# Kernel optimization log

Hardware: AMD Instinct MI355X
Metric: run time of the kernel (lower is better)

The kernel has to match this reference:

```python
import jax, jax.numpy as jnp
import numpy as np

DIM = 256
HEADS = 4
HEAD_DIM = DIM // HEADS  # 64
SCALE = (DIM / HEADS) ** -0.5
EPS = 1e-5


def layer_norm(x, g, b):
    mu = jnp.mean(x, axis=-1, keepdims=True)
    var = jnp.mean(jnp.square(x - mu), axis=-1, keepdims=True)
    return (x - mu) * jax.lax.rsqrt(var + EPS) * g + b


def setup_inputs() -> dict:
    key = jax.random.key(0)
    ks = jax.random.split(key, 8)
    B, N, C = 2, 64 * 64, DIM
    H = 4 * DIM  # mlp hidden
    s = lambda fan: 1.0 / np.sqrt(fan)
    return {
        "x": jax.random.normal(ks[0], (B, N, C), jnp.float32),
        "w_qkv": jax.random.normal(ks[1], (C, 3 * C), jnp.float32) * s(C),
        "w_ao": jax.random.normal(ks[2], (C, C), jnp.float32) * s(C),
        "b_ao": jnp.zeros((C,), jnp.float32),
        "g_ao": jnp.ones((C,), jnp.float32),
        "be_ao": jnp.zeros((C,), jnp.float32),
        "g1": jnp.ones((C,), jnp.float32),
        "be1": jnp.zeros((C,), jnp.float32),
        "w_fc1": jax.random.normal(ks[3], (C, H), jnp.float32) * s(C),
        "b_fc1": jnp.zeros((H,), jnp.float32),
        "w_fc2": jax.random.normal(ks[4], (H, C), jnp.float32) * s(H),
        "b_fc2": jnp.zeros((C,), jnp.float32),
        "g2": jnp.ones((C,), jnp.float32),
        "be2": jnp.zeros((C,), jnp.float32),
    }


def reference(x, w_qkv, w_ao, b_ao, g_ao, be_ao, g1, be1,
              w_fc1, b_fc1, w_fc2, b_fc2, g2, be2):
    b, n, c = x.shape
    shortcut = x

    # --- LinearAttention ---
    qkv = x @ w_qkv  # [b, n, 3c]
    qkv = qkv.reshape(b, n, 3, HEADS, HEAD_DIM).transpose(2, 0, 3, 1, 4)  # [3,b,h,n,d]
    q, k, v = qkv[0], qkv[1], qkv[2]
    k = jax.nn.softmax(k, axis=-2)  # softmax over sequence dim
    q = q * SCALE
    context = jnp.einsum('bhid,bhjd->bhij', k, v)   # [b,h,n,n]
    out = jnp.einsum('bhij,bhid->bhjd', context, q)  # [b,h,n,d]
    out = out.reshape(b, n, c)  # faithful to torch reshape (no transpose)
    attn_out = layer_norm(out @ w_ao + b_ao, g_ao, be_ao)

    # --- block residuals ---
    h = shortcut + layer_norm(attn_out, g1, be1)
    mlp = jax.nn.gelu(h @ w_fc1 + b_fc1) @ w_fc2 + b_fc2
    h = h + layer_norm(mlp, g2, be2)
    return shortcut + h
```

## Files before the change

kernel.cpp:

```cpp
#include <hip/hip_runtime.h>

typedef __attribute__((ext_vector_type(8))) short short8;
typedef __attribute__((ext_vector_type(4))) float f32x4;

#define EPSF 1e-5f
#define NSEQ 4096
#define R_TOT 8192

__device__ __forceinline__ float bf2f(unsigned short u){
  union { unsigned int i; float f; } v; v.i = ((unsigned int)u) << 16; return v.f;
}
__device__ __forceinline__ unsigned short f2bf(float f){
  union { float f; unsigned int i; } v; v.f = f;
  unsigned int u = v.i;
  u += 0x7FFFu + ((u >> 16) & 1u);
  return (unsigned short)(u >> 16);
}
__device__ __forceinline__ float wsum(float v){
  #pragma unroll
  for (int o = 32; o > 0; o >>= 1) v += __shfl_xor(v, o, 64);
  return v;
}
__device__ __forceinline__ float gelu_tanh(float x){
  float y = 0.7978845608028654f * (x + 0.044715f * x * x * x);
  float e = __expf(2.0f * y);
  float th = 1.0f - 2.0f / (e + 1.0f);
  return 0.5f * x * (1.0f + th);
}
__device__ __forceinline__ void gload_lds16(const unsigned short* g, unsigned short* l){
  __builtin_amdgcn_global_load_lds(
      (const __attribute__((address_space(1))) unsigned int*)g,
      (__attribute__((address_space(3))) unsigned int*)l, 16, 0, 0);
}

__global__ void k_prep(const float* __restrict__ x, unsigned short* __restrict__ xbf,
                       const float* __restrict__ w_qkv, const float* __restrict__ w_ao,
                       const float* __restrict__ w_fc1, const float* __restrict__ w_fc2,
                       unsigned short* __restrict__ oq, unsigned short* __restrict__ oa,
                       unsigned short* __restrict__ o1, unsigned short* __restrict__ o2)
{
  int bid = blockIdx.x;
  const int t = threadIdx.x;
  if (bid < 2048){
    int i = (bid * 256 + t) * 4;
    float4 v = *(const float4*)(x + i);
    ushort4 o;
    o.x = f2bf(v.x); o.y = f2bf(v.y); o.z = f2bf(v.z); o.w = f2bf(v.w);
    *(ushort4*)(xbf + i) = o;
    return;
  }
  bid -= 2048;
  const float* in; unsigned short* out; int rows, cols, tid;
  if (bid < 48)      { in = w_qkv; out = oq; rows = 256;  cols = 768;  tid = bid; }
  else if (bid < 64) { in = w_ao;  out = oa; rows = 256;  cols = 256;  tid = bid - 48; }
  else if (bid < 128){ in = w_fc1; out = o1; rows = 256;  cols = 1024; tid = bid - 64; }
  else               { in = w_fc2; out = o2; rows = 1024; cols = 256;  tid = bid - 128; }
  const int tC = cols >> 6;
  const int r0 = (tid / tC) * 64, c0 = (tid % tC) * 64;
  __shared__ float tile[64][68];
  const int i = t >> 4, j4 = (t & 15) * 4;
  #pragma unroll
  for (int p = 0; p < 4; p++){
    float4 v = *(const float4*)(in + (size_t)(r0 + i + p * 16) * cols + c0 + j4);
    tile[i + p * 16][j4 + 0] = v.x; tile[i + p * 16][j4 + 1] = v.y;
    tile[i + p * 16][j4 + 2] = v.z; tile[i + p * 16][j4 + 3] = v.w;
  }
  __syncthreads();
  #pragma unroll
  for (int p = 0; p < 4; p++){
    int ci = i + p * 16;
    ushort4 o;
    o.x = f2bf(tile[j4 + 0][ci]); o.y = f2bf(tile[j4 + 1][ci]);
    o.z = f2bf(tile[j4 + 2][ci]); o.w = f2bf(tile[j4 + 3][ci]);
    *(ushort4*)(out + (size_t)(c0 + ci) * rows + r0 + j4) = o;
  }
}

template<int BM, int BN, bool HAS_BIAS, bool DO_GELU, bool OUT_BF16>
__global__ __launch_bounds__(256) void k_gemm(const unsigned short* __restrict__ A,
                       const unsigned short* __restrict__ BT,
                       const float* __restrict__ bias,
                       float* __restrict__ Cf,
                       unsigned short* __restrict__ Cb,
                       int M, int N, int K)
{
  constexpr int BK = 64;
  constexpr int FM = BM / 32, FN = BN / 32;
  __shared__ unsigned short As[2][BM * BK];
  __shared__ unsigned short Bs[2][BN * BK];
  const int t  = threadIdx.x;
  const int l  = t & 63;
  const int w  = t >> 6;
  const int wm = w >> 1, wn = w & 1;
  const int lr = l & 15, kq = l >> 4;
  const int m0 = blockIdx.y * BM, n0 = blockIdx.x * BN;

  f32x4 acc[FM][FN];
  #pragma unroll
  for (int i = 0; i < FM; i++)
    #pragma unroll
    for (int j = 0; j < FN; j++) acc[i][j] = (f32x4){0.f, 0.f, 0.f, 0.f};

  const int crow = l >> 3, ccolE = (l & 7) * 8;
  const int nk = K / BK;

  auto stage = [&](int s, int bsel){
    #pragma unroll
    for (int c = w; c < BM / 8; c += 4)
      gload_lds16(A  + (size_t)(m0 + c * 8 + crow) * K + s * BK + ccolE, &As[bsel][c * 512]);
    #pragma unroll
    for (int c = w; c < BN / 8; c += 4)
      gload_lds16(BT + (size_t)(n0 + c * 8 + crow) * K + s * BK + ccolE, &Bs[bsel][c * 512]);
  };

  stage(0, 0);
  __syncthreads();
  for (int s = 0; s < nk; ++s){
    const int cur = s & 1;
    if (s + 1 < nk) stage(s + 1, cur ^ 1);
    #pragma unroll
    for (int kk = 0; kk < BK; kk += 32){
      short8 af[FM], bfr[FN];
      #pragma unroll
      for (int i = 0; i < FM; i++)
        af[i]  = *(const short8*)&As[cur][(wm * (BM / 2) + i * 16 + lr) * 64 + kk + kq * 8];
      #pragma unroll
      for (int j = 0; j < FN; j++)
        bfr[j] = *(const short8*)&Bs[cur][(wn * (BN / 2) + j * 16 + lr) * 64 + kk + kq * 8];
      #pragma unroll
      for (int i = 0; i < FM; i++)
        #pragma unroll
        for (int j = 0; j < FN; j++)
          acc[i][j] = __builtin_amdgcn_mfma_f32_16x16x32_bf16(af[i], bfr[j], acc[i][j], 0, 0, 0);
    }
    __syncthreads();
  }

  const int row0 = m0 + wm * (BM / 2);
  const int col0 = n0 + wn * (BN / 2);
  #pragma unroll
  for (int i = 0; i < FM; i++){
    #pragma unroll
    for (int j = 0; j < FN; j++){
      #pragma unroll
      for (int r = 0; r < 4; r++){
        int row = row0 + i * 16 + kq * 4 + r;
        int col = col0 + j * 16 + lr;
        float v = acc[i][j][r];
        if (HAS_BIAS) v += bias[col];
        if (DO_GELU)  v = gelu_tanh(v);
        if (OUT_BF16) Cb[(size_t)row * N + col] = f2bf(v);
        else          Cf[(size_t)row * N + col] = v;
      }
    }
  }
}

#define NPAD 72
__global__ __launch_bounds__(256) void k_msum(const unsigned short* __restrict__ qkv,
                                              float* __restrict__ Spart,
                                              float* __restrict__ dsum_part)
{
  __shared__ unsigned short kT[64 * NPAD];
  __shared__ unsigned short qT[80 * NPAD];
  const int t = threadIdx.x;
  const int sl = blockIdx.x;
  const int bh = blockIdx.y;
  const int b = bh >> 2, h = bh & 3;
  const int e4 = (t & 15) * 4;
  const int col = (t >> 4) * 4;
  {
    int n = sl * 64 + col;
    const unsigned short* rp = qkv + (size_t)(b * NSEQ + n) * 768 + h * 64 + e4;
    ushort4 q0 = *(const ushort4*)(rp);
    ushort4 q1 = *(const ushort4*)(rp + 768);
    ushort4 q2 = *(const ushort4*)(rp + 1536);
    ushort4 q3 = *(const ushort4*)(rp + 2304);
    ushort4 k0 = *(const ushort4*)(rp + 256);
    ushort4 k1 = *(const ushort4*)(rp + 1024);
    ushort4 k2 = *(const ushort4*)(rp + 1792);
    ushort4 k3 = *(const ushort4*)(rp + 2560);
    ushort4 w;
    w.x = q0.x; w.y = q1.x; w.z = q2.x; w.w = q3.x; *(ushort4*)&qT[(e4+0)*NPAD + col] = w;
    w.x = q0.y; w.y = q1.y; w.z = q2.y; w.w = q3.y; *(ushort4*)&qT[(e4+1)*NPAD + col] = w;
    w.x = q0.z; w.y = q1.z; w.z = q2.z; w.w = q3.z; *(ushort4*)&qT[(e4+2)*NPAD + col] = w;
    w.x = q0.w; w.y = q1.w; w.z = q2.w; w.w = q3.w; *(ushort4*)&qT[(e4+3)*NPAD + col] = w;
    w.x = f2bf(__expf(bf2f(k0.x))); w.y = f2bf(__expf(bf2f(k1.x)));
    w.z = f2bf(__expf(bf2f(k2.x))); w.w = f2bf(__expf(bf2f(k3.x)));
    *(ushort4*)&kT[(e4+0)*NPAD + col] = w;
    w.x = f2bf(__expf(bf2f(k0.y))); w.y = f2bf(__expf(bf2f(k1.y)));
    w.z = f2bf(__expf(bf2f(k2.y))); w.w = f2bf(__expf(bf2f(k3.y)));
    *(ushort4*)&kT[(e4+1)*NPAD + col] = w;
    w.x = f2bf(__expf(bf2f(k0.z))); w.y = f2bf(__expf(bf2f(k1.z)));
    w.z = f2bf(__expf(bf2f(k2.z))); w.w = f2bf(__expf(bf2f(k3.z)));
    *(ushort4*)&kT[(e4+2)*NPAD + col] = w;
    w.x = f2bf(__expf(bf2f(k0.w))); w.y = f2bf(__expf(bf2f(k1.w)));
    w.z = f2bf(__expf(bf2f(k2.w))); w.w = f2bf(__expf(bf2f(k3.w)));
    *(ushort4*)&kT[(e4+3)*NPAD + col] = w;
  }
  if (t < 16){
    ushort4 ones; ones.x = 0x3F80; ones.y = 0x3F80; ones.z = 0x3F80; ones.w = 0x3F80;
    *(ushort4*)&qT[64 * NPAD + t * 4] = ones;
  }
  __syncthreads();
  const int w4 = t >> 6, lr = t & 15, kq = (t >> 4) & 3;
  f32x4 acc[5];
  #pragma unroll
  for (int j = 0; j < 5; ++j) acc[j] = (f32x4){0.f, 0.f, 0.f, 0.f};
  #pragma unroll
  for (int ks = 0; ks < 2; ++ks){
    int nc = ks * 32 + kq * 8;
    short8 af = *(const short8*)&kT[(w4 * 16 + lr) * NPAD + nc];
    #pragma unroll
    for (int j = 0; j < 5; ++j){
      short8 bf = *(const short8*)&qT[(j * 16 + lr) * NPAD + nc];
      acc[j] = __builtin_amdgcn_mfma_f32_16x16x32_bf16(af, bf, acc[j], 0, 0, 0);
    }
  }
  float* sp = Spart + ((size_t)sl * 8 + bh) * 4096;
  #pragma unroll
  for (int j = 0; j < 4; ++j)
    #pragma unroll
    for (int r = 0; r < 4; ++r)
      sp[(w4 * 16 + kq * 4 + r) * 64 + j * 16 + lr] = acc[j][r];
  if (lr == 0){
    float* dp = dsum_part + (sl * 8 + bh) * 64;
    #pragma unroll
    for (int r = 0; r < 4; ++r) dp[w4 * 16 + kq * 4 + r] = acc[4][r];
  }
}

__global__ void k_mreduce(const float* __restrict__ Spart, const float* __restrict__ dsum_part,
                          float* __restrict__ Mm, float* __restrict__ dsumb){
  int bid = blockIdx.x, t = threadIdx.x;
  if (bid < 128){
    int idx = bid * 256 + t;
    float s = 0.f;
    #pragma unroll 8
    for (int sl = 0; sl < 64; ++sl) s += Spart[(size_t)sl * 32768 + idx];
    Mm[idx] = s;
  } else {
    int oi = (bid - 128) * 256 + t;
    float s = 0.f;
    #pragma unroll 8
    for (int sl = 0; sl < 64; ++sl) s += dsum_part[sl * 512 + oi];
    dsumb[oi] = s;
  }
}

__global__ __launch_bounds__(256) void k_projvm_dln(
    const unsigned short* __restrict__ qkv,
    const float* __restrict__ Mm, const float* __restrict__ dsumb,
    const unsigned short* __restrict__ waoT,
    const float* __restrict__ bias, const float* __restrict__ x,
    const float* __restrict__ g_ao, const float* __restrict__ be_ao,
    const float* __restrict__ g1, const float* __restrict__ be1,
    unsigned short* __restrict__ hbf, float* __restrict__ sxh)
{
  __shared__ __align__(16) char smem[16896 + 16384 + 8192 + 65536];
  unsigned short* As   = (unsigned short*)smem;
  unsigned short* vlds = (unsigned short*)(smem + 16896);
  unsigned short* mt   = (unsigned short*)(smem + 16896 + 16384);
  unsigned short* Bs0  = (unsigned short*)(smem + 41472);
  float*          yt   = (float*)(smem + 41472);

  const int t = threadIdx.x, l = t & 63, w = t >> 6;
  const int lr = l & 15, kq = l >> 4;
  const int m0 = blockIdx.x * 32;
  const int b = m0 >> 12, h = (m0 >> 10) & 3;
  const int bh = b * 4 + h;
  const int n0 = (m0 & 1023) * 4;
  const int crow = l >> 3, ccolE = (l & 7) * 8;

  const unsigned short* vbase = qkv + (size_t)(b * NSEQ + n0) * 768 + 512 + h * 64;
  #pragma unroll
  for (int c = w; c < 16; c += 4)
    gload_lds16(vbase + (size_t)(c * 8 + crow) * 768 + ccolE, vlds + c * 512);
  #pragma unroll
  for (int c = w; c < 32; c += 4)
    gload_lds16(waoT + (size_t)(c * 8 + crow) * 256 + ccolE, Bs0 + c * 512);
  {
    int e = t >> 2, d0 = (t & 3) * 16;
    float rdn = 0.125f / dsumb[bh * 64 + e];
    const float* mp = Mm + (size_t)bh * 4096 + e * 64 + d0;
    #pragma unroll
    for (int i = 0; i < 16; i += 4){
      float4 mv = *(const float4*)(mp + i);
      mt[(d0 + i + 0) * 64 + e] = f2bf(mv.x * rdn);
      mt[(d0 + i + 1) * 64 + e] = f2bf(mv.y * rdn);
      mt[(d0 + i + 2) * 64 + e] = f2bf(mv.z * rdn);
      mt[(d0 + i + 3) * 64 + e] = f2bf(mv.w * rdn);
    }
  }
  __syncthreads();
  {
    f32x4 vacc[2][4];
    #pragma unroll
    for (int i = 0; i < 2; i++)
      #pragma unroll
      for (int j = 0; j < 4; j++) vacc[i][j] = (f32x4){0.f, 0.f, 0.f, 0.f};
    #pragma unroll
    for (int kk = 0; kk < 64; kk += 32){
      short8 vf[2], mf[4];
      #pragma unroll
      for (int i = 0; i < 2; i++)
        vf[i] = *(const short8*)&vlds[((w * 2 + i) * 16 + lr) * 64 + kk + kq * 8];
      #pragma unroll
      for (int j = 0; j < 4; j++)
        mf[j] = *(const short8*)&mt[(j * 16 + lr) * 64 + kk + kq * 8];
      #pragma unroll
      for (int i = 0; i < 2; i++)
        #pragma unroll
        for (int j = 0; j < 4; j++)
          vacc[i][j] = __builtin_amdgcn_mfma_f32_16x16x32_bf16(vf[i], mf[j], vacc[i][j], 0, 0, 0);
    }
    #pragma unroll
    for (int i = 0; i < 2; i++)
      #pragma unroll
      for (int j = 0; j < 4; j++)
        #pragma unroll
        for (int r = 0; r < 4; r++)
          As[((w * 2 + i) * 4 + kq) * 264 + r * 64 + j * 16 + lr] = f2bf(vacc[i][j][r]);
  }
  __syncthreads();
  f32x4 acc[2][4];
  #pragma unroll
  for (int i = 0; i < 2; i++)
    #pragma unroll
    for (int j = 0; j < 4; j++) acc[i][j] = (f32x4){0.f, 0.f, 0.f, 0.f};
  for (int s = 0; s < 4; ++s){
    const int cur = s & 1;
    if (s + 1 < 4){
      unsigned short* bnxt = Bs0 + (cur ^ 1) * 16384;
      #pragma unroll
      for (int c = w; c < 32; c += 4)
        gload_lds16(waoT + (size_t)(c * 8 + crow) * 256 + (s + 1) * 64 + ccolE,
                    bnxt + c * 512);
    }
    const unsigned short* bcur = Bs0 + cur * 16384;
    #pragma unroll
    for (int kk = 0; kk < 64; kk += 32){
      short8 af[2], bfr[4];
      #pragma unroll
      for (int i = 0; i < 2; i++)
        af[i] = *(const short8*)&As[(i * 16 + lr) * 264 + s * 64 + kk + kq * 8];
      #pragma unroll
      for (int j = 0; j < 4; j++)
        bfr[j] = *(const short8*)&bcur[(w * 64 + j * 16 + lr) * 64 + kk + kq * 8];
      #pragma unroll
      for (int i = 0; i < 2; i++)
        #pragma unroll
        for (int j = 0; j < 4; j++)
          acc[i][j] = __builtin_amdgcn_mfma_f32_16x16x32_bf16(af[i], bfr[j], acc[i][j], 0, 0, 0);
    }
    __syncthreads();
  }
  #pragma unroll
  for (int i = 0; i < 2; i++)
    #pragma unroll
    for (int j = 0; j < 4; j++){
      float bv = bias[w * 64 + j * 16 + lr];
      #pragma unroll
      for (int r = 0; r < 4; r++)
        yt[(i * 16 + kq * 4 + r) * 260 + w * 64 + j * 16 + lr] = acc[i][j][r] + bv;
    }
  __syncthreads();
  const int gl = t & 63;
  #pragma unroll
  for (int rp = 0; rp < 8; rp++){
    int row = rp * 4 + (t >> 6);
    float4 v = *(const float4*)(yt + row * 260 + gl * 4);
    float mu = wsum(v.x + v.y + v.z + v.w) * 0.00390625f;
    float dx = v.x - mu, dy = v.y - mu, dz = v.z - mu, dw = v.w - mu;
    float rstd = rsqrtf(wsum(dx*dx + dy*dy + dz*dz + dw*dw) * 0.00390625f + EPSF);
    float4 ga = *(const float4*)(g_ao + gl * 4);
    float4 ba = *(const float4*)(be_ao + gl * 4);
    float zx = dx * rstd * ga.x + ba.x, zy = dy * rstd * ga.y + ba.y;
    float zz = dz * rstd * ga.z + ba.z, zw = dw * rstd * ga.w + ba.w;
    float mu2 = wsum(zx + zy + zz + zw) * 0.00390625f;
    float ex = zx - mu2, ey = zy - mu2, ez = zz - mu2, ew = zw - mu2;
    float rstd2 = rsqrtf(wsum(ex*ex + ey*ey + ez*ez + ew*ew) * 0.00390625f + EPSF);
    float4 gb = *(const float4*)(g1 + gl * 4);
    float4 bb = *(const float4*)(be1 + gl * 4);
    size_t off = (size_t)(m0 + row) * 256 + gl * 4;
    float4 xr = *(const float4*)(x + off);
    float hx = xr.x + ex * rstd2 * gb.x + bb.x;
    float hy = xr.y + ey * rstd2 * gb.y + bb.y;
    float hz = xr.z + ez * rstd2 * gb.z + bb.z;
    float hw = xr.w + ew * rstd2 * gb.w + bb.w;
    ushort4 hb; hb.x = f2bf(hx); hb.y = f2bf(hy); hb.z = f2bf(hz); hb.w = f2bf(hw);
    *(ushort4*)(hbf + off) = hb;
    float4 sv = {xr.x + hx, xr.y + hy, xr.z + hz, xr.w + hw};
    *(float4*)(sxh + off) = sv;
  }
}

__global__ __launch_bounds__(256) void k_fc2_ln(
    const unsigned short* __restrict__ A, const unsigned short* __restrict__ BT,
    const float* __restrict__ bias, const float* __restrict__ sxh,
    const float* __restrict__ g2, const float* __restrict__ be2,
    float* __restrict__ out)
{
  constexpr int K = 1024;
  __shared__ __align__(16) char smem[8192 + 65536];
  unsigned short* As0 = (unsigned short*)smem;
  unsigned short* Bs0 = (unsigned short*)(smem + 8192);
  float* yt = (float*)(smem + 8192);
  const int t = threadIdx.x, l = t & 63, w = t >> 6;
  const int lr = l & 15, kq = l >> 4;
  const int m0 = blockIdx.x * 32;
  const int crow = l >> 3, ccolE = (l & 7) * 8;
  f32x4 acc[2][4];
  #pragma unroll
  for (int i = 0; i < 2; i++)
    #pragma unroll
    for (int j = 0; j < 4; j++) acc[i][j] = (f32x4){0.f, 0.f, 0.f, 0.f};

  auto stage = [&](int s, int bsel){
    gload_lds16(A + (size_t)(m0 + w * 8 + crow) * K + s * 64 + ccolE,
                As0 + bsel * 2048 + w * 512);
    unsigned short* bdst = Bs0 + bsel * 16384;
    #pragma unroll
    for (int c = w; c < 32; c += 4)
      gload_lds16(BT + (size_t)(c * 8 + crow) * K + s * 64 + ccolE, bdst + c * 512);
  };

  stage(0, 0);
  __syncthreads();
  for (int s = 0; s < 16; ++s){
    const int cur = s & 1;
    if (s + 1 < 16) stage(s + 1, cur ^ 1);
    const unsigned short* acur = As0 + cur * 2048;
    const unsigned short* bcur = Bs0 + cur * 16384;
    #pragma unroll
    for (int kk = 0; kk < 64; kk += 32){
      short8 af[2], bfr[4];
      #pragma unroll
      for (int i = 0; i < 2; i++)
        af[i] = *(const short8*)&acur[(i * 16 + lr) * 64 + kk + kq * 8];
      #pragma unroll
      for (int j = 0; j < 4; j++)
        bfr[j] = *(const short8*)&bcur[(w * 64 + j * 16 + lr) * 64 + kk + kq * 8];
      #pragma unroll
      for (int i = 0; i < 2; i++)
        #pragma unroll
        for (int j = 0; j < 4; j++)
          acc[i][j] = __builtin_amdgcn_mfma_f32_16x16x32_bf16(af[i], bfr[j], acc[i][j], 0, 0, 0);
    }
    __syncthreads();
  }
  #pragma unroll
  for (int i = 0; i < 2; i++)
    #pragma unroll
    for (int j = 0; j < 4; j++){
      float bv = bias[w * 64 + j * 16 + lr];
      #pragma unroll
      for (int r = 0; r < 4; r++)
        yt[(i * 16 + kq * 4 + r) * 260 + w * 64 + j * 16 + lr] = acc[i][j][r] + bv;
    }
  __syncthreads();
  const int gl = t & 63;
  #pragma unroll
  for (int rp = 0; rp < 8; rp++){
    int row = rp * 4 + (t >> 6);
    float4 v = *(const float4*)(yt + row * 260 + gl * 4);
    float mu = wsum(v.x + v.y + v.z + v.w) * 0.00390625f;
    float dx = v.x - mu, dy = v.y - mu, dz = v.z - mu, dw = v.w - mu;
    float rstd = rsqrtf(wsum(dx*dx + dy*dy + dz*dz + dw*dw) * 0.00390625f + EPSF);
    float4 g = *(const float4*)(g2 + gl * 4);
    float4 be = *(const float4*)(be2 + gl * 4);
    size_t off = (size_t)(m0 + row) * 256 + gl * 4;
    float4 sv = *(const float4*)(sxh + off);
    float4 o;
    o.x = sv.x + dx * rstd * g.x + be.x;
    o.y = sv.y + dy * rstd * g.y + be.y;
    o.z = sv.z + dz * rstd * g.z + be.z;
    o.w = sv.w + dw * rstd * g.w + be.w;
    *(float4*)(out + off) = o;
  }
}

extern "C" void kernel_launch(void* const* d_in, const int* in_sizes, int n_in,
                              void* d_out, int out_size, void* d_ws, size_t ws_size,
                              hipStream_t stream)
{
  const float* x     = (const float*)d_in[0];
  const float* w_qkv = (const float*)d_in[1];
  const float* w_ao  = (const float*)d_in[2];
  const float* b_ao  = (const float*)d_in[3];
  const float* g_ao  = (const float*)d_in[4];
  const float* be_ao = (const float*)d_in[5];
  const float* g1    = (const float*)d_in[6];
  const float* be1   = (const float*)d_in[7];
  const float* w_fc1 = (const float*)d_in[8];
  const float* b_fc1 = (const float*)d_in[9];
  const float* w_fc2 = (const float*)d_in[10];
  const float* b_fc2 = (const float*)d_in[11];
  const float* g2    = (const float*)d_in[12];
  const float* be2   = (const float*)d_in[13];
  float* out = (float*)d_out;
  char* ws = (char*)d_ws;

  unsigned short* qkv   = (unsigned short*)(ws + 0);
  unsigned short* xbf   = (unsigned short*)(ws + 12582912);
  unsigned short* wqkvT = (unsigned short*)(ws + 16777216);
  unsigned short* waoT  = (unsigned short*)(ws + 17170432);
  unsigned short* wfc1T = (unsigned short*)(ws + 17301504);
  unsigned short* wfc2T = (unsigned short*)(ws + 17825792);
  float* Spart = (float*)(ws + 18350080);
  float* dsum_part = (float*)(ws + 26738688);
  float* Mm    = (float*)(ws + 26869760);
  float* dsumb = (float*)(ws + 27000832);
  float* sxh   = (float*)(ws + 27004928);
  unsigned short* mlp1 = (unsigned short*)(ws + 35393536);

  k_prep<<<2240, 256, 0, stream>>>(x, xbf, w_qkv, w_ao, w_fc1, w_fc2,
                                   wqkvT, waoT, wfc1T, wfc2T);

  k_gemm<128, 128, false, false, true><<<dim3(6, 64), 256, 0, stream>>>(
      xbf, wqkvT, nullptr, nullptr, qkv, R_TOT, 768, 256);

  k_msum<<<dim3(64, 8), 256, 0, stream>>>(qkv, Spart, dsum_part);
  k_mreduce<<<130, 256, 0, stream>>>(Spart, dsum_part, Mm, dsumb);

  k_projvm_dln<<<256, 256, 0, stream>>>(qkv, Mm, dsumb, waoT, b_ao, x,
                                        g_ao, be_ao, g1, be1, xbf, sxh);

  k_gemm<128, 128, true, true, true><<<dim3(8, 64), 256, 0, stream>>>(
      xbf, wfc1T, b_fc1, nullptr, mlp1, R_TOT, 1024, 256);

  k_fc2_ln<<<256, 256, 0, stream>>>(mlp1, wfc2T, b_fc2, sxh, g2, be2, out);
}
```

Measured before the change: 77.98 us.

## Fuse MLP fc1+GELU+fc2+LN into one kernel and drop the reduction kernel

The fc1 GEMM with GELU is merged into the fc2+LayerNorm kernel, so each 32-row tile keeps its 1024-wide hidden activation in LDS instead of writing it to global memory and reading it back. The k_msum kernel now loops over 4 chunks per block (16 slices instead of 64). The separate k_mreduce kernel is removed, and its partial sums are folded into k_projvm_dln. This cuts two launches and the global round trip of the MLP intermediate. In exchange, the fused kernel uses about 148KB of LDS with only 256 blocks, which lowers occupancy and parallelism, and every projection block redundantly re-reads 16 partial slices.

```diff
diff --git a/kernel.cpp b/kernel.cpp
--- a/kernel.cpp
+++ b/kernel.cpp
@@ -76,11 +76,9 @@
   }
 }
 
-template<int BM, int BN, bool HAS_BIAS, bool DO_GELU, bool OUT_BF16>
+template<int BM, int BN>
 __global__ __launch_bounds__(256) void k_gemm(const unsigned short* __restrict__ A,
                        const unsigned short* __restrict__ BT,
-                       const float* __restrict__ bias,
-                       float* __restrict__ Cf,
                        unsigned short* __restrict__ Cb,
                        int M, int N, int K)
 {
@@ -139,21 +137,15 @@
   const int row0 = m0 + wm * (BM / 2);
   const int col0 = n0 + wn * (BN / 2);
   #pragma unroll
-  for (int i = 0; i < FM; i++){
-    #pragma unroll
-    for (int j = 0; j < FN; j++){
+  for (int i = 0; i < FM; i++)
+    #pragma unroll
+    for (int j = 0; j < FN; j++)
       #pragma unroll
       for (int r = 0; r < 4; r++){
         int row = row0 + i * 16 + kq * 4 + r;
         int col = col0 + j * 16 + lr;
-        float v = acc[i][j][r];
-        if (HAS_BIAS) v += bias[col];
-        if (DO_GELU)  v = gelu_tanh(v);
-        if (OUT_BF16) Cb[(size_t)row * N + col] = f2bf(v);
-        else          Cf[(size_t)row * N + col] = v;
+        Cb[(size_t)row * N + col] = f2bf(acc[i][j][r]);
       }
-    }
-  }
 }
 
 #define NPAD 72
@@ -169,8 +161,14 @@
   const int b = bh >> 2, h = bh & 3;
   const int e4 = (t & 15) * 4;
   const int col = (t >> 4) * 4;
-  {
-    int n = sl * 64 + col;
+  const int w4 = t >> 6, lr = t & 15, kq = (t >> 4) & 3;
+
+  f32x4 acc[5];
+  #pragma unroll
+  for (int j = 0; j < 5; ++j) acc[j] = (f32x4){0.f, 0.f, 0.f, 0.f};
+
+  for (int ch = 0; ch < 4; ++ch){
+    int n = sl * 256 + ch * 64 + col;
     const unsigned short* rp = qkv + (size_t)(b * NSEQ + n) * 768 + h * 64 + e4;
     ushort4 q0 = *(const ushort4*)(rp);
     ushort4 q1 = *(const ushort4*)(rp + 768);
@@ -180,6 +178,7 @@
     ushort4 k1 = *(const ushort4*)(rp + 1024);
     ushort4 k2 = *(const ushort4*)(rp + 1792);
     ushort4 k3 = *(const ushort4*)(rp + 2560);
+    if (ch) __syncthreads();
     ushort4 w;
     w.x = q0.x; w.y = q1.x; w.z = q2.x; w.w = q3.x; *(ushort4*)&qT[(e4+0)*NPAD + col] = w;
     w.x = q0.y; w.y = q1.y; w.z = q2.y; w.w = q3.y; *(ushort4*)&qT[(e4+1)*NPAD + col] = w;
@@ -197,24 +196,20 @@
     w.x = f2bf(__expf(bf2f(k0.w))); w.y = f2bf(__expf(bf2f(k1.w)));
     w.z = f2bf(__expf(bf2f(k2.w))); w.w = f2bf(__expf(bf2f(k3.w)));
     *(ushort4*)&kT[(e4+3)*NPAD + col] = w;
-  }
-  if (t < 16){
-    ushort4 ones; ones.x = 0x3F80; ones.y = 0x3F80; ones.z = 0x3F80; ones.w = 0x3F80;
-    *(ushort4*)&qT[64 * NPAD + t * 4] = ones;
-  }
-  __syncthreads();
-  const int w4 = t >> 6, lr = t & 15, kq = (t >> 4) & 3;
-  f32x4 acc[5];
-  #pragma unroll
-  for (int j = 0; j < 5; ++j) acc[j] = (f32x4){0.f, 0.f, 0.f, 0.f};
-  #pragma unroll
-  for (int ks = 0; ks < 2; ++ks){
-    int nc = ks * 32 + kq * 8;
-    short8 af = *(const short8*)&kT[(w4 * 16 + lr) * NPAD + nc];
-    #pragma unroll
-    for (int j = 0; j < 5; ++j){
-      short8 bf = *(const short8*)&qT[(j * 16 + lr) * NPAD + nc];
-      acc[j] = __builtin_amdgcn_mfma_f32_16x16x32_bf16(af, bf, acc[j], 0, 0, 0);
+    if (ch == 0 && t < 16){
+      ushort4 ones; ones.x = 0x3F80; ones.y = 0x3F80; ones.z = 0x3F80; ones.w = 0x3F80;
+      *(ushort4*)&qT[64 * NPAD + t * 4] = ones;
+    }
+    __syncthreads();
+    #pragma unroll
+    for (int ks = 0; ks < 2; ++ks){
+      int nc = ks * 32 + kq * 8;
+      short8 af = *(const short8*)&kT[(w4 * 16 + lr) * NPAD + nc];
+      #pragma unroll
+      for (int j = 0; j < 5; ++j){
+        short8 bf = *(const short8*)&qT[(j * 16 + lr) * NPAD + nc];
+        acc[j] = __builtin_amdgcn_mfma_f32_16x16x32_bf16(af, bf, acc[j], 0, 0, 0);
+      }
     }
   }
   float* sp = Spart + ((size_t)sl * 8 + bh) * 4096;
@@ -230,27 +225,9 @@
   }
 }
 
-__global__ void k_mreduce(const float* __restrict__ Spart, const float* __restrict__ dsum_part,
-                          float* __restrict__ Mm, float* __restrict__ dsumb){
-  int bid = blockIdx.x, t = threadIdx.x;
-  if (bid < 128){
-    int idx = bid * 256 + t;
-    float s = 0.f;
-    #pragma unroll 8
-    for (int sl = 0; sl < 64; ++sl) s += Spart[(size_t)sl * 32768 + idx];
-    Mm[idx] = s;
-  } else {
-    int oi = (bid - 128) * 256 + t;
-    float s = 0.f;
-    #pragma unroll 8
-    for (int sl = 0; sl < 64; ++sl) s += dsum_part[sl * 512 + oi];
-    dsumb[oi] = s;
-  }
-}
-
 __global__ __launch_bounds__(256) void k_projvm_dln(
     const unsigned short* __restrict__ qkv,
-    const float* __restrict__ Mm, const float* __restrict__ dsumb,
+    const float* __restrict__ Spart, const float* __restrict__ dsum_part,
     const unsigned short* __restrict__ waoT,
     const float* __restrict__ bias, const float* __restrict__ x,
     const float* __restrict__ g_ao, const float* __restrict__ be_ao,
@@ -281,11 +258,18 @@
     gload_lds16(waoT + (size_t)(c * 8 + crow) * 256 + ccolE, Bs0 + c * 512);
   {
     int e = t >> 2, d0 = (t & 3) * 16;
-    float rdn = 0.125f / dsumb[bh * 64 + e];
-    const float* mp = Mm + (size_t)bh * 4096 + e * 64 + d0;
+    float dn = 0.f;
+    #pragma unroll
+    for (int sl = 0; sl < 16; ++sl) dn += dsum_part[(sl * 8 + bh) * 64 + e];
+    float rdn = 0.125f / dn;
     #pragma unroll
     for (int i = 0; i < 16; i += 4){
-      float4 mv = *(const float4*)(mp + i);
+      float4 mv = {0.f, 0.f, 0.f, 0.f};
+      #pragma unroll
+      for (int sl = 0; sl < 16; ++sl){
+        float4 p = *(const float4*)(Spart + ((size_t)sl * 8 + bh) * 4096 + e * 64 + d0 + i);
+        mv.x += p.x; mv.y += p.y; mv.z += p.z; mv.w += p.w;
+      }
       mt[(d0 + i + 0) * 64 + e] = f2bf(mv.x * rdn);
       mt[(d0 + i + 1) * 64 + e] = f2bf(mv.y * rdn);
       mt[(d0 + i + 2) * 64 + e] = f2bf(mv.z * rdn);
@@ -395,68 +379,130 @@
   }
 }
 
-__global__ __launch_bounds__(256) void k_fc2_ln(
-    const unsigned short* __restrict__ A, const unsigned short* __restrict__ BT,
-    const float* __restrict__ bias, const float* __restrict__ sxh,
+__global__ __launch_bounds__(256) void k_mlp(
+    const unsigned short* __restrict__ hbf,
+    const unsigned short* __restrict__ wfc1T, const float* __restrict__ b1,
+    const unsigned short* __restrict__ wfc2T, const float* __restrict__ b2,
+    const float* __restrict__ sxh,
     const float* __restrict__ g2, const float* __restrict__ be2,
     float* __restrict__ out)
 {
-  constexpr int K = 1024;
-  __shared__ __align__(16) char smem[8192 + 65536];
-  unsigned short* As0 = (unsigned short*)smem;
-  unsigned short* Bs0 = (unsigned short*)(smem + 8192);
-  float* yt = (float*)(smem + 8192);
+  __shared__ __align__(16) char smem[16896 + 66048 + 65536];
+  unsigned short* hAp    = (unsigned short*)smem;
+  unsigned short* hidden = (unsigned short*)(smem + 16896);
+  unsigned short* Bs0    = (unsigned short*)(smem + 16896 + 66048);
+  float* yt = (float*)(smem + 16896 + 66048);
+
   const int t = threadIdx.x, l = t & 63, w = t >> 6;
   const int lr = l & 15, kq = l >> 4;
   const int m0 = blockIdx.x * 32;
   const int crow = l >> 3, ccolE = (l & 7) * 8;
-  f32x4 acc[2][4];
+
+  auto stage = [&](int s, int bsel){
+    unsigned short* bdst = Bs0 + bsel * 16384;
+    if (s < 16){
+      int nch = s >> 2, ks = s & 3;
+      #pragma unroll
+      for (int c = w; c < 32; c += 4)
+        gload_lds16(wfc1T + (size_t)(nch * 256 + c * 8 + crow) * 256 + ks * 64 + ccolE,
+                    bdst + c * 512);
+    } else {
+      int ks = s - 16;
+      #pragma unroll
+      for (int c = w; c < 32; c += 4)
+        gload_lds16(wfc2T + (size_t)(c * 8 + crow) * 1024 + ks * 64 + ccolE,
+                    bdst + c * 512);
+    }
+  };
+
+  stage(0, 0);
+  {
+    int r = t >> 3, c0 = (t & 7) * 32;
+    const unsigned short* src = hbf + (size_t)(m0 + r) * 256 + c0;
+    #pragma unroll
+    for (int i = 0; i < 4; i++){
+      short8 v = *(const short8*)(src + i * 8);
+      *(short8*)&hAp[r * 264 + c0 + i * 8] = v;
+    }
+  }
+  __syncthreads();
+
+  f32x4 acc1[2][4], acc2[2][4];
   #pragma unroll
   for (int i = 0; i < 2; i++)
     #pragma unroll
-    for (int j = 0; j < 4; j++) acc[i][j] = (f32x4){0.f, 0.f, 0.f, 0.f};
-
-  auto stage = [&](int s, int bsel){
-    gload_lds16(A + (size_t)(m0 + w * 8 + crow) * K + s * 64 + ccolE,
-                As0 + bsel * 2048 + w * 512);
-    unsigned short* bdst = Bs0 + bsel * 16384;
-    #pragma unroll
-    for (int c = w; c < 32; c += 4)
-      gload_lds16(BT + (size_t)(c * 8 + crow) * K + s * 64 + ccolE, bdst + c * 512);
-  };
-
-  stage(0, 0);
-  __syncthreads();
-  for (int s = 0; s < 16; ++s){
+    for (int j = 0; j < 4; j++){
+      acc1[i][j] = (f32x4){0.f, 0.f, 0.f, 0.f};
+      acc2[i][j] = (f32x4){0.f, 0.f, 0.f, 0.f};
+    }
+
+  for (int s = 0; s < 32; ++s){
     const int cur = s & 1;
-    if (s + 1 < 16) stage(s + 1, cur ^ 1);
-    const unsigned short* acur = As0 + cur * 2048;
+    if (s + 1 < 32) stage(s + 1, cur ^ 1);
     const unsigned short* bcur = Bs0 + cur * 16384;
-    #pragma unroll
-    for (int kk = 0; kk < 64; kk += 32){
-      short8 af[2], bfr[4];
-      #pragma unroll
-      for (int i = 0; i < 2; i++)
-        af[i] = *(const short8*)&acur[(i * 16 + lr) * 64 + kk + kq * 8];
-      #pragma unroll
-      for (int j = 0; j < 4; j++)
-        bfr[j] = *(const short8*)&bcur[(w * 64 + j * 16 + lr) * 64 + kk + kq * 8];
-      #pragma unroll
-      for (int i = 0; i < 2; i++)
+    if (s < 16){
+      const int ks = s & 3;
+      #pragma unroll
+      for (int kk = 0; kk < 64; kk += 32){
+        short8 af[2], bfr[4];
+        #pragma unroll
+        for (int i = 0; i < 2; i++)
+          af[i] = *(const short8*)&hAp[(i * 16 + lr) * 264 + ks * 64 + kk + kq * 8];
         #pragma unroll
         for (int j = 0; j < 4; j++)
-          acc[i][j] = __builtin_amdgcn_mfma_f32_16x16x32_bf16(af[i], bfr[j], acc[i][j], 0, 0, 0);
+          bfr[j] = *(const short8*)&bcur[(w * 64 + j * 16 + lr) * 64 + kk + kq * 8];
+        #pragma unroll
+        for (int i = 0; i < 2; i++)
+          #pragma unroll
+          for (int j = 0; j < 4; j++)
+            acc1[i][j] = __builtin_amdgcn_mfma_f32_16x16x32_bf16(af[i], bfr[j], acc1[i][j], 0, 0, 0);
+      }
+      if (ks == 3){
+        const int nch = s >> 2;
+        #pragma unroll
+        for (int j = 0; j < 4; j++){
+          int col = nch * 256 + w * 64 + j * 16 + lr;
+          float bv = b1[col];
+          #pragma unroll
+          for (int i = 0; i < 2; i++){
+            #pragma unroll
+            for (int r = 0; r < 4; r++){
+              float v = gelu_tanh(acc1[i][j][r] + bv);
+              hidden[(i * 16 + kq * 4 + r) * 1032 + col] = f2bf(v);
+            }
+            acc1[i][j] = (f32x4){0.f, 0.f, 0.f, 0.f};
+          }
+        }
+      }
+    } else {
+      const int k0 = (s - 16) * 64;
+      #pragma unroll
+      for (int kk = 0; kk < 64; kk += 32){
+        short8 af[2], bfr[4];
+        #pragma unroll
+        for (int i = 0; i < 2; i++)
+          af[i] = *(const short8*)&hidden[(i * 16 + lr) * 1032 + k0 + kk + kq * 8];
+        #pragma unroll
+        for (int j = 0; j < 4; j++)
+          bfr[j] = *(const short8*)&bcur[(w * 64 + j * 16 + lr) * 64 + kk + kq * 8];
+        #pragma unroll
+        for (int i = 0; i < 2; i++)
+          #pragma unroll
+          for (int j = 0; j < 4; j++)
+            acc2[i][j] = __builtin_amdgcn_mfma_f32_16x16x32_bf16(af[i], bfr[j], acc2[i][j], 0, 0, 0);
+      }
     }
     __syncthreads();
   }
+
   #pragma unroll
   for (int i = 0; i < 2; i++)
     #pragma unroll
     for (int j = 0; j < 4; j++){
-      float bv = bias[w * 64 + j * 16 + lr];
+      float bv = b2[w * 64 + j * 16 + lr];
       #pragma unroll
       for (int r = 0; r < 4; r++)
-        yt[(i * 16 + kq * 4 + r) * 260 + w * 64 + j * 16 + lr] = acc[i][j][r] + bv;
+        yt[(i * 16 + kq * 4 + r) * 260 + w * 64 + j * 16 + lr] = acc2[i][j][r] + bv;
     }
   __syncthreads();
   const int gl = t & 63;
@@ -508,26 +554,19 @@
   unsigned short* wfc1T = (unsigned short*)(ws + 17301504);
   unsigned short* wfc2T = (unsigned short*)(ws + 17825792);
   float* Spart = (float*)(ws + 18350080);
-  float* dsum_part = (float*)(ws + 26738688);
-  float* Mm    = (float*)(ws + 26869760);
-  float* dsumb = (float*)(ws + 27000832);
-  float* sxh   = (float*)(ws + 27004928);
-  unsigned short* mlp1 = (unsigned short*)(ws + 35393536);
+  float* dsum_part = (float*)(ws + 20447232);
+  float* sxh   = (float*)(ws + 20480000);
 
   k_prep<<<2240, 256, 0, stream>>>(x, xbf, w_qkv, w_ao, w_fc1, w_fc2,
                                    wqkvT, waoT, wfc1T, wfc2T);
 
-  k_gemm<128, 128, false, false, true><<<dim3(6, 64), 256, 0, stream>>>(
-      xbf, wqkvT, nullptr, nullptr, qkv, R_TOT, 768, 256);
-
-  k_msum<<<dim3(64, 8), 256, 0, stream>>>(qkv, Spart, dsum_part);
-  k_mreduce<<<130, 256, 0, stream>>>(Spart, dsum_part, Mm, dsumb);
-
-  k_projvm_dln<<<256, 256, 0, stream>>>(qkv, Mm, dsumb, waoT, b_ao, x,
+  k_gemm<128, 128><<<dim3(6, 64), 256, 0, stream>>>(
+      xbf, wqkvT, qkv, R_TOT, 768, 256);
+
+  k_msum<<<dim3(16, 8), 256, 0, stream>>>(qkv, Spart, dsum_part);
+
+  k_projvm_dln<<<256, 256, 0, stream>>>(qkv, Spart, dsum_part, waoT, b_ao, x,
                                         g_ao, be_ao, g1, be1, xbf, sxh);
 
-  k_gemm<128, 128, true, true, true><<<dim3(8, 64), 256, 0, stream>>>(
-      xbf, wfc1T, b_fc1, nullptr, mlp1, R_TOT, 1024, 256);
-
-  k_fc2_ln<<<256, 256, 0, stream>>>(mlp1, wfc2T, b_fc2, sxh, g2, be2, out);
-}
+  k_mlp<<<256, 256, 0, stream>>>(xbf, wfc1T, b_fc1, wfc2T, b_fc2, sxh, g2, be2, out);
+}
```

Result: slower. 88.79 us (+13.9%).

## Fold partial-sum reduction into consumer and shrink msum grid to 16 slices

Applied to the files above, without the earlier changes.

k_msum now loops over four 64-token chunks per block, so each block accumulates 256 tokens and only 16 partial sums per (batch, head) are written instead of 64. The separate k_mreduce kernel is removed, and k_projvm_dln sums the 16 partials directly while building its normalized matrix. This removes one kernel launch and most of the partial-buffer traffic. In exchange, each of the 256 projection blocks redundantly re-reads its head's 16 partials, and k_msum runs with only 128 blocks and extra barriers.

```diff
diff --git a/kernel.cpp b/kernel.cpp
--- a/kernel.cpp
+++ b/kernel.cpp
@@ -169,8 +169,14 @@
   const int b = bh >> 2, h = bh & 3;
   const int e4 = (t & 15) * 4;
   const int col = (t >> 4) * 4;
-  {
-    int n = sl * 64 + col;
+  const int w4 = t >> 6, lr = t & 15, kq = (t >> 4) & 3;
+
+  f32x4 acc[5];
+  #pragma unroll
+  for (int j = 0; j < 5; ++j) acc[j] = (f32x4){0.f, 0.f, 0.f, 0.f};
+
+  for (int ch = 0; ch < 4; ++ch){
+    int n = sl * 256 + ch * 64 + col;
     const unsigned short* rp = qkv + (size_t)(b * NSEQ + n) * 768 + h * 64 + e4;
     ushort4 q0 = *(const ushort4*)(rp);
     ushort4 q1 = *(const ushort4*)(rp + 768);
@@ -180,6 +186,7 @@
     ushort4 k1 = *(const ushort4*)(rp + 1024);
     ushort4 k2 = *(const ushort4*)(rp + 1792);
     ushort4 k3 = *(const ushort4*)(rp + 2560);
+    if (ch) __syncthreads();
     ushort4 w;
     w.x = q0.x; w.y = q1.x; w.z = q2.x; w.w = q3.x; *(ushort4*)&qT[(e4+0)*NPAD + col] = w;
     w.x = q0.y; w.y = q1.y; w.z = q2.y; w.w = q3.y; *(ushort4*)&qT[(e4+1)*NPAD + col] = w;
@@ -197,24 +204,20 @@
     w.x = f2bf(__expf(bf2f(k0.w))); w.y = f2bf(__expf(bf2f(k1.w)));
     w.z = f2bf(__expf(bf2f(k2.w))); w.w = f2bf(__expf(bf2f(k3.w)));
     *(ushort4*)&kT[(e4+3)*NPAD + col] = w;
-  }
-  if (t < 16){
-    ushort4 ones; ones.x = 0x3F80; ones.y = 0x3F80; ones.z = 0x3F80; ones.w = 0x3F80;
-    *(ushort4*)&qT[64 * NPAD + t * 4] = ones;
-  }
-  __syncthreads();
-  const int w4 = t >> 6, lr = t & 15, kq = (t >> 4) & 3;
-  f32x4 acc[5];
-  #pragma unroll
-  for (int j = 0; j < 5; ++j) acc[j] = (f32x4){0.f, 0.f, 0.f, 0.f};
-  #pragma unroll
-  for (int ks = 0; ks < 2; ++ks){
-    int nc = ks * 32 + kq * 8;
-    short8 af = *(const short8*)&kT[(w4 * 16 + lr) * NPAD + nc];
-    #pragma unroll
-    for (int j = 0; j < 5; ++j){
-      short8 bf = *(const short8*)&qT[(j * 16 + lr) * NPAD + nc];
-      acc[j] = __builtin_amdgcn_mfma_f32_16x16x32_bf16(af, bf, acc[j], 0, 0, 0);
+    if (ch == 0 && t < 16){
+      ushort4 ones; ones.x = 0x3F80; ones.y = 0x3F80; ones.z = 0x3F80; ones.w = 0x3F80;
+      *(ushort4*)&qT[64 * NPAD + t * 4] = ones;
+    }
+    __syncthreads();
+    #pragma unroll
+    for (int ks = 0; ks < 2; ++ks){
+      int nc = ks * 32 + kq * 8;
+      short8 af = *(const short8*)&kT[(w4 * 16 + lr) * NPAD + nc];
+      #pragma unroll
+      for (int j = 0; j < 5; ++j){
+        short8 bf = *(const short8*)&qT[(j * 16 + lr) * NPAD + nc];
+        acc[j] = __builtin_amdgcn_mfma_f32_16x16x32_bf16(af, bf, acc[j], 0, 0, 0);
+      }
     }
   }
   float* sp = Spart + ((size_t)sl * 8 + bh) * 4096;
@@ -230,27 +233,9 @@
   }
 }
 
-__global__ void k_mreduce(const float* __restrict__ Spart, const float* __restrict__ dsum_part,
-                          float* __restrict__ Mm, float* __restrict__ dsumb){
-  int bid = blockIdx.x, t = threadIdx.x;
-  if (bid < 128){
-    int idx = bid * 256 + t;
-    float s = 0.f;
-    #pragma unroll 8
-    for (int sl = 0; sl < 64; ++sl) s += Spart[(size_t)sl * 32768 + idx];
-    Mm[idx] = s;
-  } else {
-    int oi = (bid - 128) * 256 + t;
-    float s = 0.f;
-    #pragma unroll 8
-    for (int sl = 0; sl < 64; ++sl) s += dsum_part[sl * 512 + oi];
-    dsumb[oi] = s;
-  }
-}
-
 __global__ __launch_bounds__(256) void k_projvm_dln(
     const unsigned short* __restrict__ qkv,
-    const float* __restrict__ Mm, const float* __restrict__ dsumb,
+    const float* __restrict__ Spart, const float* __restrict__ dsum_part,
     const unsigned short* __restrict__ waoT,
     const float* __restrict__ bias, const float* __restrict__ x,
     const float* __restrict__ g_ao, const float* __restrict__ be_ao,
@@ -281,11 +266,18 @@
     gload_lds16(waoT + (size_t)(c * 8 + crow) * 256 + ccolE, Bs0 + c * 512);
   {
     int e = t >> 2, d0 = (t & 3) * 16;
-    float rdn = 0.125f / dsumb[bh * 64 + e];
-    const float* mp = Mm + (size_t)bh * 4096 + e * 64 + d0;
+    float dn = 0.f;
+    #pragma unroll
+    for (int sl = 0; sl < 16; ++sl) dn += dsum_part[(sl * 8 + bh) * 64 + e];
+    float rdn = 0.125f / dn;
     #pragma unroll
     for (int i = 0; i < 16; i += 4){
-      float4 mv = *(const float4*)(mp + i);
+      float4 mv = {0.f, 0.f, 0.f, 0.f};
+      #pragma unroll
+      for (int sl = 0; sl < 16; ++sl){
+        float4 p = *(const float4*)(Spart + ((size_t)sl * 8 + bh) * 4096 + e * 64 + d0 + i);
+        mv.x += p.x; mv.y += p.y; mv.z += p.z; mv.w += p.w;
+      }
       mt[(d0 + i + 0) * 64 + e] = f2bf(mv.x * rdn);
       mt[(d0 + i + 1) * 64 + e] = f2bf(mv.y * rdn);
       mt[(d0 + i + 2) * 64 + e] = f2bf(mv.z * rdn);
@@ -508,11 +500,9 @@
   unsigned short* wfc1T = (unsigned short*)(ws + 17301504);
   unsigned short* wfc2T = (unsigned short*)(ws + 17825792);
   float* Spart = (float*)(ws + 18350080);
-  float* dsum_part = (float*)(ws + 26738688);
-  float* Mm    = (float*)(ws + 26869760);
-  float* dsumb = (float*)(ws + 27000832);
-  float* sxh   = (float*)(ws + 27004928);
-  unsigned short* mlp1 = (unsigned short*)(ws + 35393536);
+  float* dsum_part = (float*)(ws + 20447232);
+  float* sxh   = (float*)(ws + 20480000);
+  unsigned short* mlp1 = (unsigned short*)(ws + 28868608);
 
   k_prep<<<2240, 256, 0, stream>>>(x, xbf, w_qkv, w_ao, w_fc1, w_fc2,
                                    wqkvT, waoT, wfc1T, wfc2T);
@@ -520,10 +510,9 @@
   k_gemm<128, 128, false, false, true><<<dim3(6, 64), 256, 0, stream>>>(
       xbf, wqkvT, nullptr, nullptr, qkv, R_TOT, 768, 256);
 
-  k_msum<<<dim3(64, 8), 256, 0, stream>>>(qkv, Spart, dsum_part);
-  k_mreduce<<<130, 256, 0, stream>>>(Spart, dsum_part, Mm, dsumb);
-
-  k_projvm_dln<<<256, 256, 0, stream>>>(qkv, Mm, dsumb, waoT, b_ao, x,
+  k_msum<<<dim3(16, 8), 256, 0, stream>>>(qkv, Spart, dsum_part);
+
+  k_projvm_dln<<<256, 256, 0, stream>>>(qkv, Spart, dsum_part, waoT, b_ao, x,
                                         g_ao, be_ao, g1, be1, xbf, sxh);
 
   k_gemm<128, 128, true, true, true><<<dim3(8, 64), 256, 0, stream>>>(
```

Measured after the change: 80.54 us. 3.3% more time.
